# Kernel tuning notes

Measured on AMD Instinct MI355X. Metric: run time of the kernel, lower is better.

Reference implementation:

```python
import jax, jax.numpy as jnp
import numpy as np

BN_EPS = 1e-5


def setup_inputs() -> dict:
    key = jax.random.key(0)
    ks = jax.random.split(key, 6)
    P, D_IN, H, N_NODES = 2_000_000, 3, 128, 20_000
    x = jax.random.normal(ks[0], (P, D_IN), dtype=jnp.float32)
    batch_idx = jax.random.randint(ks[1], (P,), 0, N_NODES, dtype=jnp.int64)
    W1 = jax.random.normal(ks[2], (D_IN, H), dtype=jnp.float32) * 0.5
    b1 = jax.random.normal(ks[3], (H,), dtype=jnp.float32) * 0.1
    gamma = jnp.ones((H,), dtype=jnp.float32)
    beta = jnp.zeros((H,), dtype=jnp.float32)
    running_mean = jnp.zeros((H,), dtype=jnp.float32)
    running_var = jnp.ones((H,), dtype=jnp.float32)
    W2 = jax.random.normal(ks[4], (H, H), dtype=jnp.float32) * (1.0 / np.sqrt(H))
    b2 = jax.random.normal(ks[5], (H,), dtype=jnp.float32) * 0.1
    return {"x": x, "batch_idx": batch_idx, "num_nodes": N_NODES,
            "W1": W1, "b1": b1, "gamma": gamma, "beta": beta,
            "running_mean": running_mean, "running_var": running_var,
            "W2": W2, "b2": b2}


def reference(x, batch_idx, num_nodes, W1, b1, gamma, beta,
              running_mean, running_var, W2, b2):
    # per-point MLP: Linear -> BatchNorm1d (eval: running stats) -> ReLU -> Linear -> ReLU
    h = x @ W1 + b1                                        # [P, H]
    h = (h - running_mean) * jax.lax.rsqrt(running_var + BN_EPS) * gamma + beta
    h = jax.nn.relu(h)
    h = jax.nn.relu(h @ W2 + b2)                            # [P, H], values >= 0
    # scatter_max by node; torch_scatter fills empty segments with 0,
    # and since h >= 0 post-ReLU, clamping the -inf fill to 0 is exact.
    node_feats = jax.ops.segment_max(h, batch_idx, num_segments=num_nodes)
    return jnp.maximum(node_feats, 0.0)                     # [num_nodes, H]
```

## Files before the change

kernel.cpp:

```cpp
#include <hip/hip_runtime.h>
#include <hip/hip_bf16.h>

#define H 128
#define TILE_PTS 32
#define ROW_STRIDE 136
#define NBLK 192
#define BT 1024
#define BSH 4
#define NPB (1 << BSH)
#define CAP 2560

typedef __attribute__((ext_vector_type(8))) short short8;
typedef __attribute__((ext_vector_type(4))) float float4v;
typedef __attribute__((ext_vector_type(2))) float float2v;

static __device__ __forceinline__ unsigned short f2bf(float f) {
    unsigned u = __float_as_uint(f);
    unsigned r = (u + 0x7fffu + ((u >> 16) & 1u)) >> 16;
    return (unsigned short)r;
}
static __device__ __forceinline__ unsigned pkbf(float a, float b) {
    __hip_bfloat162 h = __float22bfloat162_rn(float2{a, b});
    return *reinterpret_cast<unsigned*>(&h);
}
static __device__ __forceinline__ unsigned short f2h(float f) {
    _Float16 h = (_Float16)f;
    unsigned short u;
    __builtin_memcpy(&u, &h, 2);
    return u;
}
static __device__ __forceinline__ float h2f(unsigned short us) {
    _Float16 h;
    __builtin_memcpy(&h, &us, 2);
    return (float)h;
}

__global__ __launch_bounds__(BT)
void scatter_slot(const int* __restrict__ bidx, const float* __restrict__ x,
                  const float* __restrict__ W2, unsigned short* __restrict__ W2T,
                  int* __restrict__ gcnt, uint2* __restrict__ xb,
                  int P, int nbuk) {
    extern __shared__ int lh[];
    const int b = blockIdx.x, t = threadIdx.x;
    for (int i = b * BT + t; i < H * H; i += NBLK * BT) {
        int n = i >> 7, k = i & 127;
        W2T[i] = f2bf(W2[k * H + n]);
    }
    for (int i = t; i < nbuk; i += BT) lh[i] = 0;
    __syncthreads();
    const int chunk = (P + NBLK - 1) / NBLK;
    const int lo = b * chunk;
    const int hi = (lo + chunk < P) ? lo + chunk : P;
    for (int p = lo + t; p < hi; p += BT)
        atomicAdd(&lh[bidx[p] >> BSH], 1);
    __syncthreads();
    for (int i = t; i < nbuk; i += BT) {
        int c = lh[i];
        lh[i] = (c > 0) ? atomicAdd(&gcnt[i], c) : 0;
    }
    __syncthreads();
    for (int p = lo + t; p < hi; p += BT) {
        int idx = bidx[p];
        int bk = idx >> BSH;
        int pos = atomicAdd(&lh[bk], 1);
        if (pos < CAP) {
            float x0 = x[p * 3 + 0], x1 = x[p * 3 + 1], x2 = x[p * 3 + 2];
            uint2 r;
            r.x = (unsigned)f2h(x0) | ((unsigned)f2h(x1) << 16);
            r.y = (unsigned)f2h(x2) | ((unsigned)(idx & (NPB - 1)) << 16);
            xb[(size_t)bk * CAP + pos] = r;
        }
    }
}

__global__ __launch_bounds__(256, 4)
void node_kernel7(const uint2* __restrict__ xb, const int* __restrict__ gcnt,
                  const float* __restrict__ W1, const float* __restrict__ b1,
                  const float* __restrict__ gamma, const float* __restrict__ beta,
                  const float* __restrict__ rmean, const float* __restrict__ rvar,
                  const unsigned short* __restrict__ W2T, const float* __restrict__ b2,
                  float* __restrict__ out, int N)
{
    __shared__ __align__(16) uint2 srt[CAP + TILE_PTS];
    __shared__ __align__(16) unsigned short h1s[2][TILE_PTS * ROW_STRIDE];
    __shared__ int basec[NPB + 1];
    __shared__ int cur[NPB];

    const int bk   = blockIdx.x;
    const int t    = threadIdx.x;
    const int lane = t & 63;
    const int wave = t >> 6;
    const int g  = t & 15;
    const int q  = t >> 4;
    const int c0 = g * 8;

    float2v w1f2[3][4], b1f2[4];
    #pragma unroll
    for (int jp = 0; jp < 4; ++jp) {
        #pragma unroll
        for (int e = 0; e < 2; ++e) {
            int c = c0 + 2 * jp + e;
            float sc = gamma[c] * rsqrtf(rvar[c] + 1e-5f);
            w1f2[0][jp][e] = W1[0 * H + c] * sc;
            w1f2[1][jp][e] = W1[1 * H + c] * sc;
            w1f2[2][jp][e] = W1[2 * H + c] * sc;
            b1f2[jp][e]    = (b1[c] - rmean[c]) * sc + beta[c];
        }
    }

    const int bn = lane & 15;
    const int kq = (lane >> 4) * 8;
    short8 bfrag[2][4];
    float  b2v[2];
    #pragma unroll
    for (int nt = 0; nt < 2; ++nt) {
        const int nn = wave * 32 + nt * 16 + bn;
        b2v[nt] = b2[nn];
        #pragma unroll
        for (int kk = 0; kk < 4; ++kk)
            bfrag[nt][kk] = *(const short8*)&W2T[nn * H + kk * 32 + kq];
    }

    int n_b = gcnt[bk];
    if (n_b > CAP) n_b = CAP;
    if (t < NPB) cur[t] = 0;
    __syncthreads();
    const uint2* src = xb + (size_t)bk * CAP;
    for (int p = t; p < n_b; p += 256)
        atomicAdd(&cur[src[p].y >> 16], 1);
    __syncthreads();
    if (t == 0) {
        int run = 0;
        #pragma unroll
        for (int i = 0; i < NPB; ++i) { int c = cur[i]; basec[i] = run; run += c; }
        basec[NPB] = run;
    }
    __syncthreads();
    if (t < NPB) cur[t] = basec[t];
    __syncthreads();
    for (int p = t; p < n_b; p += 256) {
        uint2 r = src[p];
        int pos = atomicAdd(&cur[r.y >> 16], 1);
        srt[pos] = r;
    }
    for (int p = n_b + t; p < n_b + TILE_PTS; p += 256) srt[p] = uint2{0u, 0u};
    __syncthreads();

    const float4v zero4 = {0.f, 0.f, 0.f, 0.f};
    const float NEG_INF = -__builtin_inff();
    const float2v zero2 = {0.f, 0.f};
    const int nodebase = bk << BSH;
    const int nlocal = (N - nodebase < NPB) ? (N - nodebase) : NPB;

    for (int j = 0; j < nlocal; ++j) {
        const int start = basec[j];
        const int n     = basec[j + 1] - start;
        const int ntiles = (n + TILE_PTS - 1) >> 5;

        float2v vmax2[2];
        vmax2[0] = float2v{NEG_INF, NEG_INF};
        vmax2[1] = float2v{NEG_INF, NEG_INF};

        auto loadx = [&](int tb, float xv[2][3]) {
            #pragma unroll
            for (int i = 0; i < 2; ++i) {
                uint2 r = srt[start + tb + q + 16 * i];
                xv[i][0] = h2f((unsigned short)(r.x & 0xffffu));
                xv[i][1] = h2f((unsigned short)(r.x >> 16));
                xv[i][2] = h2f((unsigned short)(r.y & 0xffffu));
            }
        };
        auto stage = [&](const float xv[2][3], unsigned short* buf) {
            #pragma unroll
            for (int i = 0; i < 2; ++i) {
                const int pl = q + 16 * i;
                float2v a0 = {xv[i][0], xv[i][0]};
                float2v a1 = {xv[i][1], xv[i][1]};
                float2v a2 = {xv[i][2], xv[i][2]};
                union { unsigned u[4]; short8 v; } pk;
                #pragma unroll
                for (int jp = 0; jp < 4; ++jp) {
                    float2v h = b1f2[jp];
                    h = __builtin_elementwise_fma(a0, w1f2[0][jp], h);
                    h = __builtin_elementwise_fma(a1, w1f2[1][jp], h);
                    h = __builtin_elementwise_fma(a2, w1f2[2][jp], h);
                    h = __builtin_elementwise_max(h, zero2);
                    pk.u[jp] = pkbf(h[0], h[1]);
                }
                *(short8*)&buf[pl * ROW_STRIDE + c0] = pk.v;
            }
        };

        if (ntiles > 0) {
            float xv[2][3];
            loadx(0, xv);
            stage(xv, h1s[0]);
            __syncthreads();

            int pb = 0;
            for (int tile = 0; tile < ntiles; ++tile) {
                const int tb = tile * TILE_PTS;
                const bool havenext = (tile + 1 < ntiles);

                float nx[2][3];
                if (havenext) loadx(tb + TILE_PTS, nx);

                float4v acc[2][2];
                const unsigned short* hb = h1s[pb];
                {
                    short8 a0 = *(const short8*)&hb[bn * ROW_STRIDE + kq];
                    short8 a1 = *(const short8*)&hb[(16 + bn) * ROW_STRIDE + kq];
                    #pragma unroll
                    for (int nt = 0; nt < 2; ++nt) {
                        acc[0][nt] = __builtin_amdgcn_mfma_f32_16x16x32_bf16(a0, bfrag[nt][0], zero4, 0, 0, 0);
                        acc[1][nt] = __builtin_amdgcn_mfma_f32_16x16x32_bf16(a1, bfrag[nt][0], zero4, 0, 0, 0);
                    }
                }
                #pragma unroll
                for (int kk = 1; kk < 4; ++kk) {
                    short8 a0 = *(const short8*)&hb[bn * ROW_STRIDE + kk * 32 + kq];
                    short8 a1 = *(const short8*)&hb[(16 + bn) * ROW_STRIDE + kk * 32 + kq];
                    #pragma unroll
                    for (int nt = 0; nt < 2; ++nt) {
                        acc[0][nt] = __builtin_amdgcn_mfma_f32_16x16x32_bf16(a0, bfrag[nt][kk], acc[0][nt], 0, 0, 0);
                        acc[1][nt] = __builtin_amdgcn_mfma_f32_16x16x32_bf16(a1, bfrag[nt][kk], acc[1][nt], 0, 0, 0);
                    }
                }

                if (havenext) stage(nx, h1s[pb ^ 1]);

                if (tb + TILE_PTS <= n) {
                    #pragma unroll
                    for (int ps = 0; ps < 2; ++ps)
                        #pragma unroll
                        for (int nt = 0; nt < 2; ++nt) {
                            vmax2[nt] = __builtin_elementwise_max(vmax2[nt],
                                          float2v{acc[ps][nt][0], acc[ps][nt][1]});
                            vmax2[nt] = __builtin_elementwise_max(vmax2[nt],
                                          float2v{acc[ps][nt][2], acc[ps][nt][3]});
                        }
                } else {
                    #pragma unroll
                    for (int ps = 0; ps < 2; ++ps)
                        #pragma unroll
                        for (int r = 0; r < 4; ++r) {
                            const int pl = ps * 16 + (lane >> 4) * 4 + r;
                            const bool valid = (tb + pl) < n;
                            vmax2[0][r & 1] = fmaxf(vmax2[0][r & 1], valid ? acc[ps][0][r] : NEG_INF);
                            vmax2[1][r & 1] = fmaxf(vmax2[1][r & 1], valid ? acc[ps][1][r] : NEG_INF);
                        }
                }
                __syncthreads();
                pb ^= 1;
            }
        }

        float vmax0 = fmaxf(vmax2[0][0], vmax2[0][1]);
        float vmax1 = fmaxf(vmax2[1][0], vmax2[1][1]);
        vmax0 = fmaxf(vmax0, __shfl_xor(vmax0, 16, 64));
        vmax0 = fmaxf(vmax0, __shfl_xor(vmax0, 32, 64));
        vmax1 = fmaxf(vmax1, __shfl_xor(vmax1, 16, 64));
        vmax1 = fmaxf(vmax1, __shfl_xor(vmax1, 32, 64));
        if (lane < 16) {
            float* orow = out + (size_t)(nodebase + j) * H + wave * 32;
            orow[lane]      = fmaxf(vmax0 + b2v[0], 0.f);
            orow[16 + lane] = fmaxf(vmax1 + b2v[1], 0.f);
        }
    }
}

__global__ void histB_kernel(const int* __restrict__ bidx, int* __restrict__ counts, int P) {
    int p = blockIdx.x * 256 + threadIdx.x;
    if (p < P) atomicAdd(&counts[bidx[p]], 1);
}
__global__ __launch_bounds__(1024)
void scanB_kernel(const int* __restrict__ counts, int* __restrict__ starts,
                  int* __restrict__ cursor, int N) {
    __shared__ int sums[1024];
    const int t = threadIdx.x;
    const int chunk = (N + 1023) >> 10;
    const int lo = t * chunk;
    const int hi = (lo + chunk < N) ? lo + chunk : N;
    int s = 0;
    for (int i = lo; i < hi; ++i) s += counts[i];
    sums[t] = s;
    __syncthreads();
    #pragma unroll
    for (int off = 1; off < 1024; off <<= 1) {
        int a = (t >= off) ? sums[t - off] : 0;
        __syncthreads();
        sums[t] += a;
        __syncthreads();
    }
    int run = sums[t] - s;
    for (int i = lo; i < hi; ++i) { starts[i] = run; cursor[i] = run; run += counts[i]; }
    if (t == 1023) starts[N] = sums[1023];
}
__global__ void scatterB_kernel(const int* __restrict__ bidx, const float* __restrict__ x,
                                int* __restrict__ cursor, uint2* __restrict__ xs, int P) {
    int p = blockIdx.x * 256 + threadIdx.x;
    if (p < P) {
        int pos = atomicAdd(&cursor[bidx[p]], 1);
        uint2 r;
        r.x = (unsigned)f2h(x[p * 3 + 0]) | ((unsigned)f2h(x[p * 3 + 1]) << 16);
        r.y = (unsigned)f2h(x[p * 3 + 2]);
        xs[pos] = r;
    }
}
__global__ void convw2_kernel(const float* __restrict__ W2, unsigned short* __restrict__ W2T) {
    int i = blockIdx.x * 256 + threadIdx.x;
    if (i < H * H) {
        int n = i >> 7, k = i & 127;
        W2T[i] = f2bf(W2[k * H + n]);
    }
}

__global__ __launch_bounds__(256, 4)
void node_kernelB(const uint2* __restrict__ xs,
                  const int*   __restrict__ starts,
                  const float* __restrict__ W1, const float* __restrict__ b1,
                  const float* __restrict__ gamma, const float* __restrict__ beta,
                  const float* __restrict__ rmean, const float* __restrict__ rvar,
                  const unsigned short* __restrict__ W2T, const float* __restrict__ b2,
                  float* __restrict__ out, int N)
{
    __shared__ __align__(16) unsigned short h1s[2][TILE_PTS * ROW_STRIDE];
    const int t = threadIdx.x, lane = t & 63, wave = t >> 6;
    const int g = t & 15, q = t >> 4, c0 = g * 8;
    float2v w1f2[3][4], b1f2[4];
    #pragma unroll
    for (int jp = 0; jp < 4; ++jp)
        #pragma unroll
        for (int e = 0; e < 2; ++e) {
            int c = c0 + 2 * jp + e;
            float sc = gamma[c] * rsqrtf(rvar[c] + 1e-5f);
            w1f2[0][jp][e] = W1[0 * H + c] * sc;
            w1f2[1][jp][e] = W1[1 * H + c] * sc;
            w1f2[2][jp][e] = W1[2 * H + c] * sc;
            b1f2[jp][e]    = (b1[c] - rmean[c]) * sc + beta[c];
        }
    const int bn = lane & 15, kq = (lane >> 4) * 8;
    short8 bfrag[2][4]; float b2v[2];
    #pragma unroll
    for (int nt = 0; nt < 2; ++nt) {
        const int nn = wave * 32 + nt * 16 + bn;
        b2v[nt] = b2[nn];
        #pragma unroll
        for (int kk = 0; kk < 4; ++kk)
            bfrag[nt][kk] = *(const short8*)&W2T[nn * H + kk * 32 + kq];
    }
    const float4v zero4 = {0.f, 0.f, 0.f, 0.f};
    const float NEG_INF = -__builtin_inff();
    const float2v zero2 = {0.f, 0.f};
    for (int node = blockIdx.x; node < N; node += gridDim.x) {
        const int start = starts[node];
        const int n = starts[node + 1] - start;
        const int ntiles = (n + TILE_PTS - 1) >> 5;
        float2v vmax2[2];
        vmax2[0] = float2v{NEG_INF, NEG_INF};
        vmax2[1] = float2v{NEG_INF, NEG_INF};
        auto loadx = [&](int tb, float xv[2][3]) {
            #pragma unroll
            for (int i = 0; i < 2; ++i) {
                uint2 r = xs[start + tb + q + 16 * i];
                xv[i][0] = h2f((unsigned short)(r.x & 0xffffu));
                xv[i][1] = h2f((unsigned short)(r.x >> 16));
                xv[i][2] = h2f((unsigned short)(r.y & 0xffffu));
            }
        };
        auto stage = [&](const float xv[2][3], unsigned short* buf) {
            #pragma unroll
            for (int i = 0; i < 2; ++i) {
                const int pl = q + 16 * i;
                float2v a0 = {xv[i][0], xv[i][0]};
                float2v a1 = {xv[i][1], xv[i][1]};
                float2v a2 = {xv[i][2], xv[i][2]};
                union { unsigned u[4]; short8 v; } pk;
                #pragma unroll
                for (int jp = 0; jp < 4; ++jp) {
                    float2v h = b1f2[jp];
                    h = __builtin_elementwise_fma(a0, w1f2[0][jp], h);
                    h = __builtin_elementwise_fma(a1, w1f2[1][jp], h);
                    h = __builtin_elementwise_fma(a2, w1f2[2][jp], h);
                    h = __builtin_elementwise_max(h, zero2);
                    pk.u[jp] = pkbf(h[0], h[1]);
                }
                *(short8*)&buf[pl * ROW_STRIDE + c0] = pk.v;
            }
        };
        if (ntiles > 0) {
            float xv[2][3];
            loadx(0, xv);
            stage(xv, h1s[0]);
            __syncthreads();
            int pb = 0;
            for (int tile = 0; tile < ntiles; ++tile) {
                const int tb = tile * TILE_PTS;
                const bool havenext = (tile + 1 < ntiles);
                float nx[2][3];
                if (havenext) loadx(tb + TILE_PTS, nx);
                float4v acc[2][2];
                const unsigned short* hb = h1s[pb];
                {
                    short8 a0 = *(const short8*)&hb[bn * ROW_STRIDE + kq];
                    short8 a1 = *(const short8*)&hb[(16 + bn) * ROW_STRIDE + kq];
                    #pragma unroll
                    for (int nt = 0; nt < 2; ++nt) {
                        acc[0][nt] = __builtin_amdgcn_mfma_f32_16x16x32_bf16(a0, bfrag[nt][0], zero4, 0, 0, 0);
                        acc[1][nt] = __builtin_amdgcn_mfma_f32_16x16x32_bf16(a1, bfrag[nt][0], zero4, 0, 0, 0);
                    }
                }
                #pragma unroll
                for (int kk = 1; kk < 4; ++kk) {
                    short8 a0 = *(const short8*)&hb[bn * ROW_STRIDE + kk * 32 + kq];
                    short8 a1 = *(const short8*)&hb[(16 + bn) * ROW_STRIDE + kk * 32 + kq];
                    #pragma unroll
                    for (int nt = 0; nt < 2; ++nt) {
                        acc[0][nt] = __builtin_amdgcn_mfma_f32_16x16x32_bf16(a0, bfrag[nt][kk], acc[0][nt], 0, 0, 0);
                        acc[1][nt] = __builtin_amdgcn_mfma_f32_16x16x32_bf16(a1, bfrag[nt][kk], acc[1][nt], 0, 0, 0);
                    }
                }
                if (havenext) stage(nx, h1s[pb ^ 1]);
                if (tb + TILE_PTS <= n) {
                    #pragma unroll
                    for (int ps = 0; ps < 2; ++ps)
                        #pragma unroll
                        for (int nt = 0; nt < 2; ++nt) {
                            vmax2[nt] = __builtin_elementwise_max(vmax2[nt],
                                          float2v{acc[ps][nt][0], acc[ps][nt][1]});
                            vmax2[nt] = __builtin_elementwise_max(vmax2[nt],
                                          float2v{acc[ps][nt][2], acc[ps][nt][3]});
                        }
                } else {
                    #pragma unroll
                    for (int ps = 0; ps < 2; ++ps)
                        #pragma unroll
                        for (int r = 0; r < 4; ++r) {
                            const int pl = ps * 16 + (lane >> 4) * 4 + r;
                            const bool valid = (tb + pl) < n;
                            vmax2[0][r & 1] = fmaxf(vmax2[0][r & 1], valid ? acc[ps][0][r] : NEG_INF);
                            vmax2[1][r & 1] = fmaxf(vmax2[1][r & 1], valid ? acc[ps][1][r] : NEG_INF);
                        }
                }
                __syncthreads();
                pb ^= 1;
            }
        }
        float vmax0 = fmaxf(vmax2[0][0], vmax2[0][1]);
        float vmax1 = fmaxf(vmax2[1][0], vmax2[1][1]);
        vmax0 = fmaxf(vmax0, __shfl_xor(vmax0, 16, 64));
        vmax0 = fmaxf(vmax0, __shfl_xor(vmax0, 32, 64));
        vmax1 = fmaxf(vmax1, __shfl_xor(vmax1, 16, 64));
        vmax1 = fmaxf(vmax1, __shfl_xor(vmax1, 32, 64));
        if (lane < 16) {
            float* orow = out + (size_t)node * H + wave * 32;
            orow[lane]      = fmaxf(vmax0 + b2v[0], 0.f);
            orow[16 + lane] = fmaxf(vmax1 + b2v[1], 0.f);
        }
    }
}

extern "C" void kernel_launch(void* const* d_in, const int* in_sizes, int n_in,
                              void* d_out, int out_size, void* d_ws, size_t ws_size,
                              hipStream_t stream) {
    const float* x     = (const float*)d_in[0];
    const int*   bidx  = (const int*)  d_in[1];
    const float* W1    = (const float*)d_in[3];
    const float* b1    = (const float*)d_in[4];
    const float* gamma = (const float*)d_in[5];
    const float* beta  = (const float*)d_in[6];
    const float* rmean = (const float*)d_in[7];
    const float* rvar  = (const float*)d_in[8];
    const float* W2    = (const float*)d_in[9];
    const float* b2    = (const float*)d_in[10];
    float* out = (float*)d_out;

    const int P = in_sizes[1];
    const int N = out_size / H;
    const int nbuk = (N + NPB - 1) >> BSH;

    const size_t szW2T = 32768;
    const size_t szG   = (size_t)4 * ((nbuk + 63) & ~63);
    const size_t szXb  = (size_t)8 * CAP * nbuk;
    const size_t needA = szW2T + szG + szXb + 256;
    const size_t lds1  = (size_t)4 * nbuk;

    char* w = (char*)d_ws;

    if (lds1 <= 60000 && ws_size >= needA) {
        unsigned short* W2T = (unsigned short*)w;
        int* gcnt = (int*)(w + szW2T);
        uint2* xb = (uint2*)(w + szW2T + szG);

        hipMemsetAsync(gcnt, 0, (size_t)nbuk * sizeof(int), stream);
        scatter_slot<<<NBLK, BT, lds1, stream>>>(bidx, x, W2, W2T, gcnt, xb, P, nbuk);
        node_kernel7<<<nbuk, 256, 0, stream>>>(xb, gcnt, W1, b1, gamma, beta,
                                               rmean, rvar, W2T, b2, out, N);
        return;
    }

    const int Npad = (N + 63) & ~63;
    const size_t szStarts = (size_t)4 * (Npad + 64);
    const size_t szCnt    = (size_t)4 * Npad;
    const size_t szRec    = (size_t)8 * (P + 64);
    const size_t needB    = szStarts + szW2T + 2 * szCnt + szRec + 256;
    if (ws_size >= needB) {
        int* starts = (int*)w;
        unsigned short* W2T = (unsigned short*)(w + szStarts);
        int* counts = (int*)(w + szStarts + szW2T);
        int* cursor = (int*)(w + szStarts + szW2T + szCnt);
        uint2* xs   = (uint2*)(w + szStarts + szW2T + 2 * szCnt);

        hipMemsetAsync(counts, 0, (size_t)N * sizeof(int), stream);
        const int pblocks = (P + 255) / 256;
        const int grid = (N < 2048) ? N : 2048;
        convw2_kernel<<<(H * H + 255) / 256, 256, 0, stream>>>(W2, W2T);
        histB_kernel<<<pblocks, 256, 0, stream>>>(bidx, counts, P);
        scanB_kernel<<<1, 1024, 0, stream>>>(counts, starts, cursor, N);
        scatterB_kernel<<<pblocks, 256, 0, stream>>>(bidx, x, cursor, xs, P);
        node_kernelB<<<grid, 256, 0, stream>>>(xs, starts, W1, b1, gamma, beta,
                                               rmean, rvar, W2T, b2, out, N);
    }
}
```

Baseline: 249.0 us.

## Replace per-node sorting with LDS atomicMax scatter over whole bucket tiles

The node kernel no longer counting-sorts each bucket's points by node and loops node by node. It now streams the whole bucket in 32-point tiles and reduces each output via integer atomicMax into a per-bucket LDS table of 16 nodes by 128 columns. This is valid because outputs are non-negative after ReLU, and it removes the sort passes and the partially filled tail tiles each node used to waste. Each wave now covers 16 points by 64 columns, so bias and ReLU are applied before the max. The scatter kernel also reads batch indices and x with 16-byte vector loads, and occupancy drops to 3 blocks per CU with more LDS atomics per tile.

```diff
diff --git a/kernel.cpp b/kernel.cpp
--- a/kernel.cpp
+++ b/kernel.cpp
@@ -9,10 +9,12 @@
 #define BSH 4
 #define NPB (1 << BSH)
 #define CAP 2560
+#define CROW 132
 
 typedef __attribute__((ext_vector_type(8))) short short8;
 typedef __attribute__((ext_vector_type(4))) float float4v;
 typedef __attribute__((ext_vector_type(2))) float float2v;
+typedef __attribute__((ext_vector_type(4))) int int4v;
 
 static __device__ __forceinline__ unsigned short f2bf(float f) {
     unsigned u = __float_as_uint(f);
@@ -48,43 +50,63 @@
     }
     for (int i = t; i < nbuk; i += BT) lh[i] = 0;
     __syncthreads();
-    const int chunk = (P + NBLK - 1) / NBLK;
-    const int lo = b * chunk;
-    const int hi = (lo + chunk < P) ? lo + chunk : P;
-    for (int p = lo + t; p < hi; p += BT)
-        atomicAdd(&lh[bidx[p] >> BSH], 1);
+    const int chunk4 = (((P + NBLK - 1) / NBLK) + 3) & ~3;
+    const int lo = b * chunk4;
+    const int hi = (lo + chunk4 < P) ? lo + chunk4 : P;
+    for (int p4 = lo + 4 * t; p4 < hi; p4 += 4 * BT) {
+        if (p4 + 4 <= hi) {
+            int4v i4 = *(const int4v*)&bidx[p4];
+            atomicAdd(&lh[i4.x >> BSH], 1);
+            atomicAdd(&lh[i4.y >> BSH], 1);
+            atomicAdd(&lh[i4.z >> BSH], 1);
+            atomicAdd(&lh[i4.w >> BSH], 1);
+        } else {
+            for (int p = p4; p < hi; ++p) atomicAdd(&lh[bidx[p] >> BSH], 1);
+        }
+    }
     __syncthreads();
     for (int i = t; i < nbuk; i += BT) {
         int c = lh[i];
         lh[i] = (c > 0) ? atomicAdd(&gcnt[i], c) : 0;
     }
     __syncthreads();
-    for (int p = lo + t; p < hi; p += BT) {
-        int idx = bidx[p];
-        int bk = idx >> BSH;
-        int pos = atomicAdd(&lh[bk], 1);
+    auto emit = [&](int idx, float x0, float x1, float x2) {
+        int pos = atomicAdd(&lh[idx >> BSH], 1);
         if (pos < CAP) {
-            float x0 = x[p * 3 + 0], x1 = x[p * 3 + 1], x2 = x[p * 3 + 2];
             uint2 r;
             r.x = (unsigned)f2h(x0) | ((unsigned)f2h(x1) << 16);
             r.y = (unsigned)f2h(x2) | ((unsigned)(idx & (NPB - 1)) << 16);
-            xb[(size_t)bk * CAP + pos] = r;
-        }
-    }
-}
-
-__global__ __launch_bounds__(256, 4)
-void node_kernel7(const uint2* __restrict__ xb, const int* __restrict__ gcnt,
+            xb[(size_t)(idx >> BSH) * CAP + pos] = r;
+        }
+    };
+    for (int p4 = lo + 4 * t; p4 < hi; p4 += 4 * BT) {
+        if (p4 + 4 <= hi) {
+            int4v i4 = *(const int4v*)&bidx[p4];
+            float4v xa = *(const float4v*)(x + (size_t)p4 * 3);
+            float4v xbv = *(const float4v*)(x + (size_t)p4 * 3 + 4);
+            float4v xc = *(const float4v*)(x + (size_t)p4 * 3 + 8);
+            emit(i4.x, xa[0], xa[1], xa[2]);
+            emit(i4.y, xa[3], xbv[0], xbv[1]);
+            emit(i4.z, xbv[2], xbv[3], xc[0]);
+            emit(i4.w, xc[1], xc[2], xc[3]);
+        } else {
+            for (int p = p4; p < hi; ++p)
+                emit(bidx[p], x[p * 3 + 0], x[p * 3 + 1], x[p * 3 + 2]);
+        }
+    }
+}
+
+__global__ __launch_bounds__(256, 3)
+void node_kernel8(const uint2* __restrict__ xb, const int* __restrict__ gcnt,
                   const float* __restrict__ W1, const float* __restrict__ b1,
                   const float* __restrict__ gamma, const float* __restrict__ beta,
                   const float* __restrict__ rmean, const float* __restrict__ rvar,
                   const unsigned short* __restrict__ W2T, const float* __restrict__ b2,
                   float* __restrict__ out, int N)
 {
-    __shared__ __align__(16) uint2 srt[CAP + TILE_PTS];
     __shared__ __align__(16) unsigned short h1s[2][TILE_PTS * ROW_STRIDE];
-    __shared__ int basec[NPB + 1];
-    __shared__ int cur[NPB];
+    __shared__ __align__(16) int nids[2][TILE_PTS];
+    __shared__ int colmax[17 * CROW];
 
     const int bk   = blockIdx.x;
     const int t    = threadIdx.x;
@@ -108,164 +130,123 @@
         }
     }
 
+    const int psub = wave >> 1;
+    const int half = wave & 1;
     const int bn = lane & 15;
     const int kq = (lane >> 4) * 8;
-    short8 bfrag[2][4];
-    float  b2v[2];
+    short8 bfrag[4][4];
+    float  b2v[4];
     #pragma unroll
-    for (int nt = 0; nt < 2; ++nt) {
-        const int nn = wave * 32 + nt * 16 + bn;
+    for (int nt = 0; nt < 4; ++nt) {
+        const int nn = half * 64 + nt * 16 + bn;
         b2v[nt] = b2[nn];
         #pragma unroll
         for (int kk = 0; kk < 4; ++kk)
             bfrag[nt][kk] = *(const short8*)&W2T[nn * H + kk * 32 + kq];
     }
 
+    for (int i = t; i < 17 * CROW; i += 256) colmax[i] = 0;
+
     int n_b = gcnt[bk];
     if (n_b > CAP) n_b = CAP;
-    if (t < NPB) cur[t] = 0;
+    const int ntile = (n_b + TILE_PTS - 1) >> 5;
+    const uint2* src = xb + (size_t)bk * CAP;
+
+    const float4v zero4 = {0.f, 0.f, 0.f, 0.f};
+    const float2v zero2 = {0.f, 0.f};
+
+    auto stage = [&](const uint2 rec[2], int buf, int tb) {
+        #pragma unroll
+        for (int i = 0; i < 2; ++i) {
+            const int pl = q + 16 * i;
+            float x0 = h2f((unsigned short)(rec[i].x & 0xffffu));
+            float x1 = h2f((unsigned short)(rec[i].x >> 16));
+            float x2 = h2f((unsigned short)(rec[i].y & 0xffffu));
+            float2v a0 = {x0, x0}, a1 = {x1, x1}, a2 = {x2, x2};
+            union { unsigned u[4]; short8 v; } pk;
+            #pragma unroll
+            for (int jp = 0; jp < 4; ++jp) {
+                float2v h = b1f2[jp];
+                h = __builtin_elementwise_fma(a0, w1f2[0][jp], h);
+                h = __builtin_elementwise_fma(a1, w1f2[1][jp], h);
+                h = __builtin_elementwise_fma(a2, w1f2[2][jp], h);
+                h = __builtin_elementwise_max(h, zero2);
+                pk.u[jp] = pkbf(h[0], h[1]);
+            }
+            *(short8*)&h1s[buf][pl * ROW_STRIDE + c0] = pk.v;
+            if (g == 0)
+                nids[buf][pl] = (tb + pl >= n_b) ? 16 : (int)(rec[i].y >> 16);
+        }
+    };
+
+    if (ntile > 0) {
+        uint2 rec[2];
+        rec[0] = src[q];
+        rec[1] = src[q + 16];
+        stage(rec, 0, 0);
+    }
     __syncthreads();
-    const uint2* src = xb + (size_t)bk * CAP;
-    for (int p = t; p < n_b; p += 256)
-        atomicAdd(&cur[src[p].y >> 16], 1);
-    __syncthreads();
-    if (t == 0) {
-        int run = 0;
-        #pragma unroll
-        for (int i = 0; i < NPB; ++i) { int c = cur[i]; basec[i] = run; run += c; }
-        basec[NPB] = run;
-    }
-    __syncthreads();
-    if (t < NPB) cur[t] = basec[t];
-    __syncthreads();
-    for (int p = t; p < n_b; p += 256) {
-        uint2 r = src[p];
-        int pos = atomicAdd(&cur[r.y >> 16], 1);
-        srt[pos] = r;
-    }
-    for (int p = n_b + t; p < n_b + TILE_PTS; p += 256) srt[p] = uint2{0u, 0u};
-    __syncthreads();
-
-    const float4v zero4 = {0.f, 0.f, 0.f, 0.f};
-    const float NEG_INF = -__builtin_inff();
-    const float2v zero2 = {0.f, 0.f};
-    const int nodebase = bk << BSH;
-    const int nlocal = (N - nodebase < NPB) ? (N - nodebase) : NPB;
-
-    for (int j = 0; j < nlocal; ++j) {
-        const int start = basec[j];
-        const int n     = basec[j + 1] - start;
-        const int ntiles = (n + TILE_PTS - 1) >> 5;
-
-        float2v vmax2[2];
-        vmax2[0] = float2v{NEG_INF, NEG_INF};
-        vmax2[1] = float2v{NEG_INF, NEG_INF};
-
-        auto loadx = [&](int tb, float xv[2][3]) {
+
+    int pb = 0;
+    for (int tile = 0; tile < ntile; ++tile) {
+        const int tb = tile * TILE_PTS;
+        const bool have = (tile + 1 < ntile);
+
+        uint2 nr[2];
+        if (have) {
+            nr[0] = src[tb + TILE_PTS + q];
+            nr[1] = src[tb + TILE_PTS + q + 16];
+        }
+
+        float4v acc[4];
+        const unsigned short* hb = h1s[pb];
+        const int arow = (psub * 16 + bn) * ROW_STRIDE;
+        {
+            short8 a = *(const short8*)&hb[arow + kq];
             #pragma unroll
-            for (int i = 0; i < 2; ++i) {
-                uint2 r = srt[start + tb + q + 16 * i];
-                xv[i][0] = h2f((unsigned short)(r.x & 0xffffu));
-                xv[i][1] = h2f((unsigned short)(r.x >> 16));
-                xv[i][2] = h2f((unsigned short)(r.y & 0xffffu));
-            }
-        };
-        auto stage = [&](const float xv[2][3], unsigned short* buf) {
+            for (int nt = 0; nt < 4; ++nt)
+                acc[nt] = __builtin_amdgcn_mfma_f32_16x16x32_bf16(a, bfrag[nt][0], zero4, 0, 0, 0);
+        }
+        #pragma unroll
+        for (int kk = 1; kk < 4; ++kk) {
+            short8 a = *(const short8*)&hb[arow + kk * 32 + kq];
             #pragma unroll
-            for (int i = 0; i < 2; ++i) {
-                const int pl = q + 16 * i;
-                float2v a0 = {xv[i][0], xv[i][0]};
-                float2v a1 = {xv[i][1], xv[i][1]};
-                float2v a2 = {xv[i][2], xv[i][2]};
-                union { unsigned u[4]; short8 v; } pk;
-                #pragma unroll
-                for (int jp = 0; jp < 4; ++jp) {
-                    float2v h = b1f2[jp];
-                    h = __builtin_elementwise_fma(a0, w1f2[0][jp], h);
-                    h = __builtin_elementwise_fma(a1, w1f2[1][jp], h);
-                    h = __builtin_elementwise_fma(a2, w1f2[2][jp], h);
-                    h = __builtin_elementwise_max(h, zero2);
-                    pk.u[jp] = pkbf(h[0], h[1]);
-                }
-                *(short8*)&buf[pl * ROW_STRIDE + c0] = pk.v;
-            }
-        };
-
-        if (ntiles > 0) {
-            float xv[2][3];
-            loadx(0, xv);
-            stage(xv, h1s[0]);
-            __syncthreads();
-
-            int pb = 0;
-            for (int tile = 0; tile < ntiles; ++tile) {
-                const int tb = tile * TILE_PTS;
-                const bool havenext = (tile + 1 < ntiles);
-
-                float nx[2][3];
-                if (havenext) loadx(tb + TILE_PTS, nx);
-
-                float4v acc[2][2];
-                const unsigned short* hb = h1s[pb];
-                {
-                    short8 a0 = *(const short8*)&hb[bn * ROW_STRIDE + kq];
-                    short8 a1 = *(const short8*)&hb[(16 + bn) * ROW_STRIDE + kq];
-                    #pragma unroll
-                    for (int nt = 0; nt < 2; ++nt) {
-                        acc[0][nt] = __builtin_amdgcn_mfma_f32_16x16x32_bf16(a0, bfrag[nt][0], zero4, 0, 0, 0);
-                        acc[1][nt] = __builtin_amdgcn_mfma_f32_16x16x32_bf16(a1, bfrag[nt][0], zero4, 0, 0, 0);
-                    }
-                }
-                #pragma unroll
-                for (int kk = 1; kk < 4; ++kk) {
-                    short8 a0 = *(const short8*)&hb[bn * ROW_STRIDE + kk * 32 + kq];
-                    short8 a1 = *(const short8*)&hb[(16 + bn) * ROW_STRIDE + kk * 32 + kq];
-                    #pragma unroll
-                    for (int nt = 0; nt < 2; ++nt) {
-                        acc[0][nt] = __builtin_amdgcn_mfma_f32_16x16x32_bf16(a0, bfrag[nt][kk], acc[0][nt], 0, 0, 0);
-                        acc[1][nt] = __builtin_amdgcn_mfma_f32_16x16x32_bf16(a1, bfrag[nt][kk], acc[1][nt], 0, 0, 0);
-                    }
-                }
-
-                if (havenext) stage(nx, h1s[pb ^ 1]);
-
-                if (tb + TILE_PTS <= n) {
-                    #pragma unroll
-                    for (int ps = 0; ps < 2; ++ps)
-                        #pragma unroll
-                        for (int nt = 0; nt < 2; ++nt) {
-                            vmax2[nt] = __builtin_elementwise_max(vmax2[nt],
-                                          float2v{acc[ps][nt][0], acc[ps][nt][1]});
-                            vmax2[nt] = __builtin_elementwise_max(vmax2[nt],
-                                          float2v{acc[ps][nt][2], acc[ps][nt][3]});
-                        }
-                } else {
-                    #pragma unroll
-                    for (int ps = 0; ps < 2; ++ps)
-                        #pragma unroll
-                        for (int r = 0; r < 4; ++r) {
-                            const int pl = ps * 16 + (lane >> 4) * 4 + r;
-                            const bool valid = (tb + pl) < n;
-                            vmax2[0][r & 1] = fmaxf(vmax2[0][r & 1], valid ? acc[ps][0][r] : NEG_INF);
-                            vmax2[1][r & 1] = fmaxf(vmax2[1][r & 1], valid ? acc[ps][1][r] : NEG_INF);
-                        }
-                }
-                __syncthreads();
-                pb ^= 1;
-            }
-        }
-
-        float vmax0 = fmaxf(vmax2[0][0], vmax2[0][1]);
-        float vmax1 = fmaxf(vmax2[1][0], vmax2[1][1]);
-        vmax0 = fmaxf(vmax0, __shfl_xor(vmax0, 16, 64));
-        vmax0 = fmaxf(vmax0, __shfl_xor(vmax0, 32, 64));
-        vmax1 = fmaxf(vmax1, __shfl_xor(vmax1, 16, 64));
-        vmax1 = fmaxf(vmax1, __shfl_xor(vmax1, 32, 64));
-        if (lane < 16) {
-            float* orow = out + (size_t)(nodebase + j) * H + wave * 32;
-            orow[lane]      = fmaxf(vmax0 + b2v[0], 0.f);
-            orow[16 + lane] = fmaxf(vmax1 + b2v[1], 0.f);
-        }
+            for (int nt = 0; nt < 4; ++nt)
+                acc[nt] = __builtin_amdgcn_mfma_f32_16x16x32_bf16(a, bfrag[nt][kk], acc[nt], 0, 0, 0);
+        }
+
+        if (have) stage(nr, pb ^ 1, tb + TILE_PTS);
+
+        int4v nid4 = *(const int4v*)&nids[pb][psub * 16 + (lane >> 4) * 4];
+        const int ccb = half * 64 + bn;
+        #pragma unroll
+        for (int nt = 0; nt < 4; ++nt) {
+            float2v bb = {b2v[nt], b2v[nt]};
+            float2v v01 = __builtin_elementwise_max(float2v{acc[nt][0], acc[nt][1]} + bb, zero2);
+            float2v v23 = __builtin_elementwise_max(float2v{acc[nt][2], acc[nt][3]} + bb, zero2);
+            const int cc = ccb + nt * 16;
+            atomicMax(&colmax[nid4.x * CROW + cc], __float_as_int(v01[0]));
+            atomicMax(&colmax[nid4.y * CROW + cc], __float_as_int(v01[1]));
+            atomicMax(&colmax[nid4.z * CROW + cc], __float_as_int(v23[0]));
+            atomicMax(&colmax[nid4.w * CROW + cc], __float_as_int(v23[1]));
+        }
+        __syncthreads();
+        pb ^= 1;
+    }
+
+    const int row = t >> 4;
+    const int node = (bk << BSH) + row;
+    if (node < N) {
+        const int c8 = (t & 15) * 8;
+        float4v v0, v1;
+        #pragma unroll
+        for (int j = 0; j < 4; ++j) {
+            v0[j] = __int_as_float(colmax[row * CROW + c8 + j]);
+            v1[j] = __int_as_float(colmax[row * CROW + c8 + 4 + j]);
+        }
+        float* orow = out + (size_t)node * H + c8;
+        *(float4v*)orow = v0;
+        *(float4v*)(orow + 4) = v1;
     }
 }
 
@@ -481,7 +462,7 @@
 
     const size_t szW2T = 32768;
     const size_t szG   = (size_t)4 * ((nbuk + 63) & ~63);
-    const size_t szXb  = (size_t)8 * CAP * nbuk;
+    const size_t szXb  = (size_t)8 * ((size_t)CAP * nbuk + 64);
     const size_t needA = szW2T + szG + szXb + 256;
     const size_t lds1  = (size_t)4 * nbuk;
 
@@ -494,7 +475,7 @@
 
         hipMemsetAsync(gcnt, 0, (size_t)nbuk * sizeof(int), stream);
         scatter_slot<<<NBLK, BT, lds1, stream>>>(bidx, x, W2, W2T, gcnt, xb, P, nbuk);
-        node_kernel7<<<nbuk, 256, 0, stream>>>(xb, gcnt, W1, b1, gamma, beta,
+        node_kernel8<<<nbuk, 256, 0, stream>>>(xb, gcnt, W1, b1, gamma, beta,
                                                rmean, rvar, W2T, b2, out, N);
         return;
     }
```

After: 242.0 us. 1.03x faster.

## Vectorize scatter loads, shrink bucket capacity, and alias raw staging with MLP buffers

Applied to the files above, without the earlier changes.

The scatter kernel now reads batch indices as int4 and x as three float4 loads per four points, with chunk bounds rounded to multiples of four; this cuts the number of global load instructions. Bucket capacity drops from 2560 to 2048 slots, which shrinks the intermediate buffer. The node kernel copies each bucket's raw records into LDS once, reusing the double-buffered hidden-activation area, and then counts and sorts from LDS instead of reading global memory twice. The smaller LDS footprint may allow more resident blocks, but any bucket holding more than 2048 points would now silently drop points.

```diff
diff --git a/kernel.cpp b/kernel.cpp
--- a/kernel.cpp
+++ b/kernel.cpp
@@ -8,11 +8,14 @@
 #define BT 1024
 #define BSH 4
 #define NPB (1 << BSH)
-#define CAP 2560
+#define CAP 2048
+#define RAWN (CAP + 32)
+#define HBUF (TILE_PTS * ROW_STRIDE)
 
 typedef __attribute__((ext_vector_type(8))) short short8;
 typedef __attribute__((ext_vector_type(4))) float float4v;
 typedef __attribute__((ext_vector_type(2))) float float2v;
+typedef __attribute__((ext_vector_type(4))) int int4v;
 
 static __device__ __forceinline__ unsigned short f2bf(float f) {
     unsigned u = __float_as_uint(f);
@@ -48,41 +51,62 @@
     }
     for (int i = t; i < nbuk; i += BT) lh[i] = 0;
     __syncthreads();
-    const int chunk = (P + NBLK - 1) / NBLK;
-    const int lo = b * chunk;
-    const int hi = (lo + chunk < P) ? lo + chunk : P;
-    for (int p = lo + t; p < hi; p += BT)
-        atomicAdd(&lh[bidx[p] >> BSH], 1);
+    const int chunk4 = (((P + NBLK - 1) / NBLK) + 3) & ~3;
+    const int lo = b * chunk4;
+    const int hi = (lo + chunk4 < P) ? lo + chunk4 : P;
+    for (int p4 = lo + 4 * t; p4 < hi; p4 += 4 * BT) {
+        if (p4 + 4 <= hi) {
+            int4v i4 = *(const int4v*)&bidx[p4];
+            atomicAdd(&lh[i4.x >> BSH], 1);
+            atomicAdd(&lh[i4.y >> BSH], 1);
+            atomicAdd(&lh[i4.z >> BSH], 1);
+            atomicAdd(&lh[i4.w >> BSH], 1);
+        } else {
+            for (int p = p4; p < hi; ++p) atomicAdd(&lh[bidx[p] >> BSH], 1);
+        }
+    }
     __syncthreads();
     for (int i = t; i < nbuk; i += BT) {
         int c = lh[i];
         lh[i] = (c > 0) ? atomicAdd(&gcnt[i], c) : 0;
     }
     __syncthreads();
-    for (int p = lo + t; p < hi; p += BT) {
-        int idx = bidx[p];
-        int bk = idx >> BSH;
-        int pos = atomicAdd(&lh[bk], 1);
+    auto emit = [&](int idx, float x0, float x1, float x2) {
+        int pos = atomicAdd(&lh[idx >> BSH], 1);
         if (pos < CAP) {
-            float x0 = x[p * 3 + 0], x1 = x[p * 3 + 1], x2 = x[p * 3 + 2];
             uint2 r;
             r.x = (unsigned)f2h(x0) | ((unsigned)f2h(x1) << 16);
             r.y = (unsigned)f2h(x2) | ((unsigned)(idx & (NPB - 1)) << 16);
-            xb[(size_t)bk * CAP + pos] = r;
+            xb[(size_t)(idx >> BSH) * CAP + pos] = r;
+        }
+    };
+    for (int p4 = lo + 4 * t; p4 < hi; p4 += 4 * BT) {
+        if (p4 + 4 <= hi) {
+            int4v i4 = *(const int4v*)&bidx[p4];
+            float4v xa = *(const float4v*)(x + (size_t)p4 * 3);
+            float4v xbv = *(const float4v*)(x + (size_t)p4 * 3 + 4);
+            float4v xc = *(const float4v*)(x + (size_t)p4 * 3 + 8);
+            emit(i4.x, xa[0], xa[1], xa[2]);
+            emit(i4.y, xa[3], xbv[0], xbv[1]);
+            emit(i4.z, xbv[2], xbv[3], xc[0]);
+            emit(i4.w, xc[1], xc[2], xc[3]);
+        } else {
+            for (int p = p4; p < hi; ++p)
+                emit(bidx[p], x[p * 3 + 0], x[p * 3 + 1], x[p * 3 + 2]);
         }
     }
 }
 
 __global__ __launch_bounds__(256, 4)
-void node_kernel7(const uint2* __restrict__ xb, const int* __restrict__ gcnt,
+void node_kernel9(const uint2* __restrict__ xb, const int* __restrict__ gcnt,
                   const float* __restrict__ W1, const float* __restrict__ b1,
                   const float* __restrict__ gamma, const float* __restrict__ beta,
                   const float* __restrict__ rmean, const float* __restrict__ rvar,
                   const unsigned short* __restrict__ W2T, const float* __restrict__ b2,
                   float* __restrict__ out, int N)
 {
-    __shared__ __align__(16) uint2 srt[CAP + TILE_PTS];
-    __shared__ __align__(16) unsigned short h1s[2][TILE_PTS * ROW_STRIDE];
+    __shared__ __align__(16) unsigned short pool[2 * HBUF];
+    __shared__ __align__(16) uint2 srt[RAWN];
     __shared__ int basec[NPB + 1];
     __shared__ int cur[NPB];
 
@@ -121,13 +145,15 @@
             bfrag[nt][kk] = *(const short8*)&W2T[nn * H + kk * 32 + kq];
     }
 
+    uint2* raw = (uint2*)pool;
     int n_b = gcnt[bk];
     if (n_b > CAP) n_b = CAP;
+    const uint2* src = xb + (size_t)bk * CAP;
+    for (int p = t; p < n_b; p += 256) raw[p] = src[p];
     if (t < NPB) cur[t] = 0;
     __syncthreads();
-    const uint2* src = xb + (size_t)bk * CAP;
     for (int p = t; p < n_b; p += 256)
-        atomicAdd(&cur[src[p].y >> 16], 1);
+        atomicAdd(&cur[raw[p].y >> 16], 1);
     __syncthreads();
     if (t == 0) {
         int run = 0;
@@ -139,11 +165,12 @@
     if (t < NPB) cur[t] = basec[t];
     __syncthreads();
     for (int p = t; p < n_b; p += 256) {
-        uint2 r = src[p];
+        uint2 r = raw[p];
         int pos = atomicAdd(&cur[r.y >> 16], 1);
         srt[pos] = r;
     }
-    for (int p = n_b + t; p < n_b + TILE_PTS; p += 256) srt[p] = uint2{0u, 0u};
+    for (int p = n_b + t; p < n_b + TILE_PTS; p += 256)
+        if (p < RAWN) srt[p] = uint2{0u, 0u};
     __syncthreads();
 
     const float4v zero4 = {0.f, 0.f, 0.f, 0.f};
@@ -152,111 +179,110 @@
     const int nodebase = bk << BSH;
     const int nlocal = (N - nodebase < NPB) ? (N - nodebase) : NPB;
 
+    const int st0 = q * ROW_STRIDE + c0;
+    const int st1 = (q + 16) * ROW_STRIDE + c0;
+    const int ar  = bn * ROW_STRIDE + kq;
+
+    #define STAGE_PT(r, hs, so)                                            \
+    {                                                                      \
+        float x0 = h2f((unsigned short)((r).x & 0xffffu));                 \
+        float x1 = h2f((unsigned short)((r).x >> 16));                     \
+        float x2 = h2f((unsigned short)((r).y & 0xffffu));                 \
+        float2v a0 = {x0, x0}, a1 = {x1, x1}, a2 = {x2, x2};               \
+        int4v pk;                                                          \
+        _Pragma("unroll")                                                  \
+        for (int jp = 0; jp < 4; ++jp) {                                   \
+            float2v hh = b1f2[jp];                                         \
+            hh = __builtin_elementwise_fma(a0, w1f2[0][jp], hh);           \
+            hh = __builtin_elementwise_fma(a1, w1f2[1][jp], hh);           \
+            hh = __builtin_elementwise_fma(a2, w1f2[2][jp], hh);           \
+            hh = __builtin_elementwise_max(hh, zero2);                     \
+            pk[jp] = (int)pkbf(hh[0], hh[1]);                              \
+        }                                                                  \
+        *(int4v*)(void*)&(hs)[so] = pk;                                    \
+    }
+
     for (int j = 0; j < nlocal; ++j) {
-        const int start = basec[j];
-        const int n     = basec[j + 1] - start;
+        const int startj = basec[j];
+        const int n      = basec[j + 1] - startj;
         const int ntiles = (n + TILE_PTS - 1) >> 5;
 
-        float2v vmax2[2];
-        vmax2[0] = float2v{NEG_INF, NEG_INF};
-        vmax2[1] = float2v{NEG_INF, NEG_INF};
-
-        auto loadx = [&](int tb, float xv[2][3]) {
-            #pragma unroll
-            for (int i = 0; i < 2; ++i) {
-                uint2 r = srt[start + tb + q + 16 * i];
-                xv[i][0] = h2f((unsigned short)(r.x & 0xffffu));
-                xv[i][1] = h2f((unsigned short)(r.x >> 16));
-                xv[i][2] = h2f((unsigned short)(r.y & 0xffffu));
+        float2v vm0 = {NEG_INF, NEG_INF};
+        float2v vm1 = {NEG_INF, NEG_INF};
+
+        if (ntiles > 0) {
+            unsigned short* hb = pool;
+            unsigned short* hs = pool + HBUF;
+            {
+                uint2 r0 = srt[startj + q];
+                uint2 r1 = srt[startj + q + 16];
+                STAGE_PT(r0, hb, st0);
+                STAGE_PT(r1, hb, st1);
             }
-        };
-        auto stage = [&](const float xv[2][3], unsigned short* buf) {
-            #pragma unroll
-            for (int i = 0; i < 2; ++i) {
-                const int pl = q + 16 * i;
-                float2v a0 = {xv[i][0], xv[i][0]};
-                float2v a1 = {xv[i][1], xv[i][1]};
-                float2v a2 = {xv[i][2], xv[i][2]};
-                union { unsigned u[4]; short8 v; } pk;
-                #pragma unroll
-                for (int jp = 0; jp < 4; ++jp) {
-                    float2v h = b1f2[jp];
-                    h = __builtin_elementwise_fma(a0, w1f2[0][jp], h);
-                    h = __builtin_elementwise_fma(a1, w1f2[1][jp], h);
-                    h = __builtin_elementwise_fma(a2, w1f2[2][jp], h);
-                    h = __builtin_elementwise_max(h, zero2);
-                    pk.u[jp] = pkbf(h[0], h[1]);
-                }
-                *(short8*)&buf[pl * ROW_STRIDE + c0] = pk.v;
-            }
-        };
-
-        if (ntiles > 0) {
-            float xv[2][3];
-            loadx(0, xv);
-            stage(xv, h1s[0]);
             __syncthreads();
 
-            int pb = 0;
             for (int tile = 0; tile < ntiles; ++tile) {
                 const int tb = tile * TILE_PTS;
-                const bool havenext = (tile + 1 < ntiles);
-
-                float nx[2][3];
-                if (havenext) loadx(tb + TILE_PTS, nx);
-
-                float4v acc[2][2];
-                const unsigned short* hb = h1s[pb];
+                const bool have = (tile + 1 < ntiles);
+
+                uint2 n0, n1;
+                if (have) {
+                    n0 = srt[startj + tb + TILE_PTS + q];
+                    n1 = srt[startj + tb + TILE_PTS + 16 + q];
+                }
+
+                float4v acc00, acc01, acc10, acc11;
                 {
-                    short8 a0 = *(const short8*)&hb[bn * ROW_STRIDE + kq];
-                    short8 a1 = *(const short8*)&hb[(16 + bn) * ROW_STRIDE + kq];
-                    #pragma unroll
-                    for (int nt = 0; nt < 2; ++nt) {
-                        acc[0][nt] = __builtin_amdgcn_mfma_f32_16x16x32_bf16(a0, bfrag[nt][0], zero4, 0, 0, 0);
-                        acc[1][nt] = __builtin_amdgcn_mfma_f32_16x16x32_bf16(a1, bfrag[nt][0], zero4, 0, 0, 0);
-                    }
+                    short8 a0v = *(const short8*)(const void*)&hb[ar];
+                    short8 a1v = *(const short8*)(const void*)&hb[ar + 16 * ROW_STRIDE];
+                    acc00 = __builtin_amdgcn_mfma_f32_16x16x32_bf16(a0v, bfrag[0][0], zero4, 0, 0, 0);
+                    acc01 = __builtin_amdgcn_mfma_f32_16x16x32_bf16(a0v, bfrag[1][0], zero4, 0, 0, 0);
+                    acc10 = __builtin_amdgcn_mfma_f32_16x16x32_bf16(a1v, bfrag[0][0], zero4, 0, 0, 0);
+                    acc11 = __builtin_amdgcn_mfma_f32_16x16x32_bf16(a1v, bfrag[1][0], zero4, 0, 0, 0);
                 }
                 #pragma unroll
                 for (int kk = 1; kk < 4; ++kk) {
-                    short8 a0 = *(const short8*)&hb[bn * ROW_STRIDE + kk * 32 + kq];
-                    short8 a1 = *(const short8*)&hb[(16 + bn) * ROW_STRIDE + kk * 32 + kq];
+                    short8 a0v = *(const short8*)(const void*)&hb[ar + kk * 32];
+                    short8 a1v = *(const short8*)(const void*)&hb[ar + 16 * ROW_STRIDE + kk * 32];
+                    acc00 = __builtin_amdgcn_mfma_f32_16x16x32_bf16(a0v, bfrag[0][kk], acc00, 0, 0, 0);
+                    acc01 = __builtin_amdgcn_mfma_f32_16x16x32_bf16(a0v, bfrag[1][kk], acc01, 0, 0, 0);
+                    acc10 = __builtin_amdgcn_mfma_f32_16x16x32_bf16(a1v, bfrag[0][kk], acc10, 0, 0, 0);
+                    acc11 = __builtin_amdgcn_mfma_f32_16x16x32_bf16(a1v, bfrag[1][kk], acc11, 0, 0, 0);
+                }
+
+                if (have) {
+                    STAGE_PT(n0, hs, st0);
+                    STAGE_PT(n1, hs, st1);
+                }
+
+                if (tb + TILE_PTS <= n) {
+                    vm0 = __builtin_elementwise_max(vm0, float2v{acc00[0], acc00[1]});
+                    vm0 = __builtin_elementwise_max(vm0, float2v{acc00[2], acc00[3]});
+                    vm0 = __builtin_elementwise_max(vm0, float2v{acc10[0], acc10[1]});
+                    vm0 = __builtin_elementwise_max(vm0, float2v{acc10[2], acc10[3]});
+                    vm1 = __builtin_elementwise_max(vm1, float2v{acc01[0], acc01[1]});
+                    vm1 = __builtin_elementwise_max(vm1, float2v{acc01[2], acc01[3]});
+                    vm1 = __builtin_elementwise_max(vm1, float2v{acc11[0], acc11[1]});
+                    vm1 = __builtin_elementwise_max(vm1, float2v{acc11[2], acc11[3]});
+                } else {
+                    const int r0base = (lane >> 4) * 4;
                     #pragma unroll
-                    for (int nt = 0; nt < 2; ++nt) {
-                        acc[0][nt] = __builtin_amdgcn_mfma_f32_16x16x32_bf16(a0, bfrag[nt][kk], acc[0][nt], 0, 0, 0);
-                        acc[1][nt] = __builtin_amdgcn_mfma_f32_16x16x32_bf16(a1, bfrag[nt][kk], acc[1][nt], 0, 0, 0);
+                    for (int r = 0; r < 4; ++r) {
+                        const bool v0 = (tb + r0base + r) < n;
+                        const bool v1 = (tb + 16 + r0base + r) < n;
+                        vm0[r & 1] = fmaxf(vm0[r & 1], v0 ? acc00[r] : NEG_INF);
+                        vm1[r & 1] = fmaxf(vm1[r & 1], v0 ? acc01[r] : NEG_INF);
+                        vm0[r & 1] = fmaxf(vm0[r & 1], v1 ? acc10[r] : NEG_INF);
+                        vm1[r & 1] = fmaxf(vm1[r & 1], v1 ? acc11[r] : NEG_INF);
                     }
                 }
-
-                if (havenext) stage(nx, h1s[pb ^ 1]);
-
-                if (tb + TILE_PTS <= n) {
-                    #pragma unroll
-                    for (int ps = 0; ps < 2; ++ps)
-                        #pragma unroll
-                        for (int nt = 0; nt < 2; ++nt) {
-                            vmax2[nt] = __builtin_elementwise_max(vmax2[nt],
-                                          float2v{acc[ps][nt][0], acc[ps][nt][1]});
-                            vmax2[nt] = __builtin_elementwise_max(vmax2[nt],
-                                          float2v{acc[ps][nt][2], acc[ps][nt][3]});
-                        }
-                } else {
-                    #pragma unroll
-                    for (int ps = 0; ps < 2; ++ps)
-                        #pragma unroll
-                        for (int r = 0; r < 4; ++r) {
-                            const int pl = ps * 16 + (lane >> 4) * 4 + r;
-                            const bool valid = (tb + pl) < n;
-                            vmax2[0][r & 1] = fmaxf(vmax2[0][r & 1], valid ? acc[ps][0][r] : NEG_INF);
-                            vmax2[1][r & 1] = fmaxf(vmax2[1][r & 1], valid ? acc[ps][1][r] : NEG_INF);
-                        }
-                }
                 __syncthreads();
-                pb ^= 1;
+                unsigned short* tmp = hb; hb = hs; hs = tmp;
             }
         }
 
-        float vmax0 = fmaxf(vmax2[0][0], vmax2[0][1]);
-        float vmax1 = fmaxf(vmax2[1][0], vmax2[1][1]);
+        float vmax0 = fmaxf(vm0[0], vm0[1]);
+        float vmax1 = fmaxf(vm1[0], vm1[1]);
         vmax0 = fmaxf(vmax0, __shfl_xor(vmax0, 16, 64));
         vmax0 = fmaxf(vmax0, __shfl_xor(vmax0, 32, 64));
         vmax1 = fmaxf(vmax1, __shfl_xor(vmax1, 16, 64));
@@ -267,6 +293,7 @@
             orow[16 + lane] = fmaxf(vmax1 + b2v[1], 0.f);
         }
     }
+    #undef STAGE_PT
 }
 
 __global__ void histB_kernel(const int* __restrict__ bidx, int* __restrict__ counts, int P) {
@@ -375,7 +402,7 @@
                 float2v a0 = {xv[i][0], xv[i][0]};
                 float2v a1 = {xv[i][1], xv[i][1]};
                 float2v a2 = {xv[i][2], xv[i][2]};
-                union { unsigned u[4]; short8 v; } pk;
+                int4v pk;
                 #pragma unroll
                 for (int jp = 0; jp < 4; ++jp) {
                     float2v h = b1f2[jp];
@@ -383,9 +410,9 @@
                     h = __builtin_elementwise_fma(a1, w1f2[1][jp], h);
                     h = __builtin_elementwise_fma(a2, w1f2[2][jp], h);
                     h = __builtin_elementwise_max(h, zero2);
-                    pk.u[jp] = pkbf(h[0], h[1]);
-                }
-                *(short8*)&buf[pl * ROW_STRIDE + c0] = pk.v;
+                    pk[jp] = (int)pkbf(h[0], h[1]);
+                }
+                *(int4v*)(void*)&buf[pl * ROW_STRIDE + c0] = pk;
             }
         };
         if (ntiles > 0) {
@@ -481,7 +508,7 @@
 
     const size_t szW2T = 32768;
     const size_t szG   = (size_t)4 * ((nbuk + 63) & ~63);
-    const size_t szXb  = (size_t)8 * CAP * nbuk;
+    const size_t szXb  = (size_t)8 * ((size_t)CAP * nbuk + 64);
     const size_t needA = szW2T + szG + szXb + 256;
     const size_t lds1  = (size_t)4 * nbuk;
 
@@ -494,7 +521,7 @@
 
         hipMemsetAsync(gcnt, 0, (size_t)nbuk * sizeof(int), stream);
         scatter_slot<<<NBLK, BT, lds1, stream>>>(bidx, x, W2, W2T, gcnt, xb, P, nbuk);
-        node_kernel7<<<nbuk, 256, 0, stream>>>(xb, gcnt, W1, b1, gamma, beta,
+        node_kernel9<<<nbuk, 256, 0, stream>>>(xb, gcnt, W1, b1, gamma, beta,
                                                rmean, rvar, W2T, b2, out, N);
         return;
     }
```

Measured after the change: 228.9 us. 8.1% less time.
